# Kernel tuning notes

Measured on AMD Instinct MI355X. Metric: run time of the kernel, lower is better.

Reference implementation:

```python
import jax, jax.numpy as jnp
import numpy as np

N, E, G = 50000, 400000, 2048
H, C = 4, 64            # heads, hidden per head
IN, ED, TASKS = 29, 6, 12
HC = H * C


def setup_inputs() -> dict:
    key = jax.random.key(0)
    ks = jax.random.split(key, 20)
    s = 0.1
    f32 = jnp.float32
    inp = {
        'x': jax.random.normal(ks[0], (N, IN), f32),
        'edge_index': jax.random.randint(ks[1], (2, E), 0, N),
        'edge_attr': jax.random.normal(ks[2], (E, ED), f32),
        'batch': jnp.sort(jax.random.randint(ks[3], (N,), 0, G)),
        # layer 1 (in=29 -> H*C=256)
        'W1': jax.random.normal(ks[4], (IN, HC), f32) * s,
        'as1': jax.random.normal(ks[5], (1, H, C), f32) * s,
        'ad1': jax.random.normal(ks[6], (1, H, C), f32) * s,
        'We1': jax.random.normal(ks[7], (ED, HC), f32) * s,
        'ae1': jax.random.normal(ks[8], (1, H, C), f32) * s,
        'b1': jnp.zeros((HC,), f32),
        # layer 2 (in=256 -> 256)
        'W2': jax.random.normal(ks[9], (HC, HC), f32) * s,
        'as2': jax.random.normal(ks[10], (1, H, C), f32) * s,
        'ad2': jax.random.normal(ks[11], (1, H, C), f32) * s,
        'We2': jax.random.normal(ks[12], (ED, HC), f32) * s,
        'ae2': jax.random.normal(ks[13], (1, H, C), f32) * s,
        'b2': jnp.zeros((HC,), f32),
        # readout linear (256 -> 12)
        'Wl': jax.random.normal(ks[14], (HC, TASKS), f32) * s,
        'bl': jnp.zeros((TASKS,), f32),
    }
    return inp


def _gat_conv(x, src, dst, eattr, W, a_src, a_dst, We, a_e, b):
    """PyG GATConv, concat=True, leaky_relu slope 0.2, self-loops already appended."""
    h = (x @ W).reshape(N, H, C)                      # [N,H,C]
    al_s = jnp.sum(h * a_src, axis=-1)                # [N,H]
    al_d = jnp.sum(h * a_dst, axis=-1)                # [N,H]
    he = (eattr @ We).reshape(-1, H, C)               # [Etot,H,C]
    al_e = jnp.sum(he * a_e, axis=-1)                 # [Etot,H]
    alpha = al_s[src] + al_d[dst] + al_e              # [Etot,H]
    alpha = jax.nn.leaky_relu(alpha, negative_slope=0.2)
    # segment softmax over incoming edges of each dst node
    amax = jax.ops.segment_max(alpha, dst, num_segments=N)
    ex = jnp.exp(alpha - amax[dst])
    denom = jax.ops.segment_sum(ex, dst, num_segments=N)
    alpha = ex / (denom[dst] + 1e-16)
    msg = h[src] * alpha[:, :, None]                  # [Etot,H,C]
    out = jax.ops.segment_sum(msg, dst, num_segments=N)
    return out.reshape(N, HC) + b


def reference(x, edge_index, edge_attr, batch,
              W1, as1, ad1, We1, ae1, b1,
              W2, as2, ad2, We2, ae2, b2, Wl, bl):
    # add self-loops with edge_attr fill = mean over existing edges (PyG default)
    loop = jnp.arange(N)
    src = jnp.concatenate([edge_index[0], loop])
    dst = jnp.concatenate([edge_index[1], loop])
    mean_e = jnp.mean(edge_attr, axis=0, keepdims=True)
    eattr = jnp.concatenate([edge_attr, jnp.broadcast_to(mean_e, (N, ED))], axis=0)

    h = _gat_conv(x, src, dst, eattr, W1, as1, ad1, We1, ae1, b1)
    h = jax.nn.relu(h)
    h = _gat_conv(h, src, dst, eattr, W2, as2, ad2, We2, ae2, b2)
    h = jax.nn.relu(h)

    # global mean pool over graphs
    sums = jax.ops.segment_sum(h, batch, num_segments=G)      # [G,HC]
    cnt = jax.ops.segment_sum(jnp.ones((N,), h.dtype), batch, num_segments=G)
    pooled = sums / jnp.maximum(cnt, 1.0)[:, None]
    return pooled @ Wl + bl
```

## Files before the change

### kernel.cpp

```cpp
#include <hip/hip_runtime.h>
#include <math.h>

static constexpr int NN = 50000;
static constexpr int EE = 400000;
static constexpr int GG = 2048;
static constexpr int TASKS = 12;

typedef __attribute__((ext_vector_type(8))) short short8;
typedef __attribute__((ext_vector_type(4))) float floatx4;

__device__ __forceinline__ unsigned short f2bf(float f) {
  unsigned u = __float_as_uint(f);
  u = u + 0x7fffu + ((u >> 16) & 1u);
  return (unsigned short)(u >> 16);
}
__device__ __forceinline__ float bflo(unsigned u) { return __uint_as_float(u << 16); }
__device__ __forceinline__ float bfhi(unsigned u) { return __uint_as_float(u & 0xffff0000u); }

static constexpr int NBDEG = (EE + 255) / 256;
static constexpr int NBMEAN = 256;
static constexpr int NBX = (NN * 4 + 255) / 256;
static constexpr int NW1 = 32;
static constexpr int NW2 = 256;
__global__ void k_pre(const int* __restrict__ dst, const float* __restrict__ ea,
                      const float* __restrict__ x, const float* __restrict__ W1,
                      const float* __restrict__ W2, int* __restrict__ deg,
                      float* __restrict__ msum, unsigned short* __restrict__ xb,
                      unsigned short* __restrict__ w1t, unsigned short* __restrict__ w2t) {
  const int b = blockIdx.x;
  const int t = threadIdx.x;
  if (b < NBDEG) {
    int e = b * 256 + t;
    if (e < EE) atomicAdd(&deg[dst[e]], 1);
  } else if (b < NBDEG + NBMEAN) {
    float s[6] = {0, 0, 0, 0, 0, 0};
    for (int e = (b - NBDEG) * 256 + t; e < EE; e += NBMEAN * 256) {
#pragma unroll
      for (int d = 0; d < 6; d++) s[d] += ea[(size_t)e * 6 + d];
    }
    __shared__ float ls[6];
    if (t < 6) ls[t] = 0.f;
    __syncthreads();
#pragma unroll
    for (int d = 0; d < 6; d++) atomicAdd(&ls[d], s[d]);
    __syncthreads();
    if (t < 6) atomicAdd(&msum[t], ls[t]);
  } else if (b < NBDEG + NBMEAN + NBX) {
    int i = (b - NBDEG - NBMEAN) * 256 + t;
    if (i < NN * 4) {
      int n = i >> 2, seg = i & 3;
      unsigned short v[8];
#pragma unroll
      for (int j = 0; j < 8; j++) {
        int k = seg * 8 + j;
        v[j] = (k < 29) ? f2bf(x[(size_t)n * 29 + k]) : (unsigned short)0;
      }
      *(short8*)(xb + (size_t)n * 32 + seg * 8) = *(short8*)v;
    }
  } else if (b < NBDEG + NBMEAN + NBX + NW1) {
    int i = (b - NBDEG - NBMEAN - NBX) * 256 + t;
    int row = i >> 5, k = i & 31;
    unsigned short v = (k < 29) ? f2bf(W1[(size_t)k * 256 + row]) : (unsigned short)0;
    w1t[((row >> 4) * 4 + (k >> 3)) * 128 + (row & 15) * 8 + (k & 7)] = v;
  } else {
    int i = (b - NBDEG - NBMEAN - NBX - NW1) * 256 + t;
    int row = i >> 8, k = i & 255;
    w2t[((row >> 4) * 32 + (k >> 3)) * 128 + (row & 15) * 8 + (k & 7)] = f2bf(W2[(size_t)k * 256 + row]);
  }
}

__global__ void k_scan1(const int* __restrict__ deg, int* __restrict__ rowptr, int* __restrict__ bsums) {
  __shared__ int sh[256];
  int i = blockIdx.x * 256 + threadIdx.x;
  int v = (i < NN) ? deg[i] : 0;
  sh[threadIdx.x] = v;
  __syncthreads();
  for (int off = 1; off < 256; off <<= 1) {
    int t = (threadIdx.x >= off) ? sh[threadIdx.x - off] : 0;
    __syncthreads();
    sh[threadIdx.x] += t;
    __syncthreads();
  }
  if (i < NN) rowptr[i] = sh[threadIdx.x] - v;
  if (threadIdx.x == 255) bsums[blockIdx.x] = sh[255];
}

__global__ void k_scan23(int* __restrict__ rowptr, const int* __restrict__ bsums, int nb) {
  __shared__ int sh[256];
  const int t = threadIdx.x;
  sh[t] = (t < nb) ? bsums[t] : 0;
  __syncthreads();
  for (int off = 1; off < 256; off <<= 1) {
    int tv = (t >= off) ? sh[t - off] : 0;
    __syncthreads();
    sh[t] += tv;
    __syncthreads();
  }
  const int add = (blockIdx.x == 0) ? 0 : sh[blockIdx.x - 1];
  int i = blockIdx.x * 256 + t;
  if (i < NN) rowptr[i] += add;
  if (i == 0) rowptr[NN] = EE;
}

template <int KP>
__device__ __forceinline__ void gemm_body(
    int bx, const unsigned short* __restrict__ A, const unsigned short* __restrict__ Bt,
    const float* __restrict__ a_s, const float* __restrict__ a_d,
    unsigned short* __restrict__ Y, float* __restrict__ als, float* __restrict__ ald, int M) {
  const int tid = threadIdx.x;
  const int lane = tid & 63;
  const int w = tid >> 6;
  const int l15 = lane & 15;
  const int quad = lane >> 4;
  const int row0 = bx * 64;

  floatx4 acc[4][4];
#pragma unroll
  for (int i = 0; i < 4; i++)
#pragma unroll
    for (int j = 0; j < 4; j++) acc[i][j] = {0.f, 0.f, 0.f, 0.f};

  const unsigned short* pa[4];
  const unsigned short* pb[4];
#pragma unroll
  for (int i = 0; i < 4; i++) {
    int r = row0 + i * 16 + l15;
    if (r >= M) r = M - 1;
    pa[i] = A + (size_t)r * KP + quad * 8;
  }
#pragma unroll
  for (int j = 0; j < 4; j++)
    pb[j] = Bt + (size_t)((w * 4 + j) * (KP / 8) + quad) * 128 + l15 * 8;

  constexpr int NPH = KP / 32;
  short8 af[2][4], bfr[2][4];
#pragma unroll
  for (int i = 0; i < 4; i++) af[0][i] = *(const short8*)pa[i];
#pragma unroll
  for (int j = 0; j < 4; j++) bfr[0][j] = *(const short8*)pb[j];
#pragma unroll
  for (int ph = 0; ph < NPH; ph++) {
    const int cur = ph & 1, nxt = cur ^ 1;
    if (ph + 1 < NPH) {
#pragma unroll
      for (int i = 0; i < 4; i++) {
        pa[i] += 32;
        af[nxt][i] = *(const short8*)pa[i];
      }
#pragma unroll
      for (int j = 0; j < 4; j++) {
        pb[j] += 512;
        bfr[nxt][j] = *(const short8*)pb[j];
      }
    }
#pragma unroll
    for (int i = 0; i < 4; i++)
#pragma unroll
      for (int j = 0; j < 4; j++)
        acc[i][j] = __builtin_amdgcn_mfma_f32_16x16x32_bf16(af[cur][i], bfr[cur][j], acc[i][j], 0, 0, 0);
  }
  float asc[4], adc[4];
#pragma unroll
  for (int j = 0; j < 4; j++) {
    asc[j] = a_s[w * 64 + j * 16 + l15];
    adc[j] = a_d[w * 64 + j * 16 + l15];
  }
#pragma unroll
  for (int i = 0; i < 4; i++) {
#pragma unroll
    for (int r = 0; r < 4; r++) {
      const int row = row0 + i * 16 + quad * 4 + r;
      unsigned ub[4];
      float hv[4];
#pragma unroll
      for (int j = 0; j < 4; j++) {
        ub[j] = f2bf(acc[i][j][r]);
        hv[j] = __uint_as_float(ub[j] << 16);
      }
      if (row < M) {
#pragma unroll
        for (int j = 0; j < 4; j++) Y[(size_t)row * 256 + w * 64 + j * 16 + l15] = (unsigned short)ub[j];
      }
      float ps = hv[0] * asc[0] + hv[1] * asc[1] + hv[2] * asc[2] + hv[3] * asc[3];
      float pd = hv[0] * adc[0] + hv[1] * adc[1] + hv[2] * adc[2] + hv[3] * adc[3];
#pragma unroll
      for (int off = 1; off < 16; off <<= 1) {
        ps += __shfl_xor(ps, off, 64);
        pd += __shfl_xor(pd, off, 64);
      }
      if (l15 == 0 && row < M) {
        als[row * 4 + w] = ps;
        ald[row * 4 + w] = pd;
      }
    }
  }
}

static constexpr int GB = (NN + 63) / 64;

__global__ __launch_bounds__(256, 2) void k_scatgemm1(
    const int* __restrict__ ei, const int* __restrict__ rowptr, int* __restrict__ cursor,
    int* __restrict__ csrc, int* __restrict__ eslot, const float* __restrict__ We1,
    const float* __restrict__ ae1, const float* __restrict__ We2, const float* __restrict__ ae2,
    const float* __restrict__ msum, float* __restrict__ p1, float* __restrict__ p2,
    const unsigned short* __restrict__ xb, const unsigned short* __restrict__ w1t,
    const float* __restrict__ as1, const float* __restrict__ ad1,
    unsigned short* __restrict__ hb, float* __restrict__ als, float* __restrict__ ald) {
  const int b = blockIdx.x;
  const int t = threadIdx.x;
  if (b < NBDEG) {
    int e = b * 256 + t;
    if (e >= EE) return;
    int s = ei[e];
    int d = ei[EE + e];
    int p = atomicAdd(&cursor[d], 1);
    int slot = rowptr[d] + p;
    csrc[slot] = s;
    eslot[e] = slot;
  } else if (b < NBDEG + 2) {
    const int layer = b - NBDEG;
    const float* We = layer ? We2 : We1;
    const float* ae = layer ? ae2 : ae1;
    float* params = layer ? p2 : p1;
    __shared__ float vsh[24];
    if (t < 24) {
      int d = t >> 2, h = t & 3;
      float s = 0.f;
      for (int c = 0; c < 64; c++) s += We[d * 256 + h * 64 + c] * ae[h * 64 + c];
      vsh[t] = s;
      params[t] = s;
    }
    __syncthreads();
    if (t < 4) {
      float s = 0.f;
      const float invE = 1.0f / (float)EE;
#pragma unroll
      for (int d = 0; d < 6; d++) s += (msum[d] * invE) * vsh[d * 4 + t];
      params[24 + t] = s;
    }
  } else {
    gemm_body<32>(b - NBDEG - 2, xb, w1t, as1, ad1, hb, als, ald, NN);
  }
}

__global__ __launch_bounds__(256, 2) void k_gemm2(
    const unsigned short* __restrict__ A, const unsigned short* __restrict__ Bt,
    const float* __restrict__ a_s, const float* __restrict__ a_d,
    unsigned short* __restrict__ Y, float* __restrict__ als, float* __restrict__ ald) {
  gemm_body<256>(blockIdx.x, A, Bt, a_s, a_d, Y, als, ald, NN);
}

__device__ __forceinline__ float leaky02(float x) { return x > 0.f ? x : 0.2f * x; }

__global__ void k_edge(const int* __restrict__ ei, const float* __restrict__ ea,
                       const float* __restrict__ als, const float* __restrict__ ald,
                       const int* __restrict__ eslot, const float* __restrict__ params,
                       float* __restrict__ exa) {
  int e = blockIdx.x * blockDim.x + threadIdx.x;
  if (e >= EE) return;
  int src = ei[e], dst = ei[EE + e];
  float4 s4 = *(const float4*)(als + (size_t)src * 4);
  float4 d4 = *(const float4*)(ald + (size_t)dst * 4);
  float ed[6];
#pragma unroll
  for (int d = 0; d < 6; d++) ed[d] = ea[(size_t)e * 6 + d];
  float sl[4] = {s4.x + d4.x, s4.y + d4.y, s4.z + d4.z, s4.w + d4.w};
  float out[4];
#pragma unroll
  for (int h = 0; h < 4; h++) {
    float x = sl[h];
#pragma unroll
    for (int d = 0; d < 6; d++) x += ed[d] * params[d * 4 + h];
    out[h] = __expf(leaky02(x));
  }
  *(float4*)(exa + (size_t)eslot[e] * 4) = make_float4(out[0], out[1], out[2], out[3]);
}

__global__ __launch_bounds__(256) void k_agg(
    const unsigned short* __restrict__ hinb, const float* __restrict__ als,
    const float* __restrict__ ald, const int* __restrict__ rowptr, const int* __restrict__ csrc,
    const float* __restrict__ exa, const float* __restrict__ params, const float* __restrict__ bias,
    unsigned short* __restrict__ houtb) {
  const int lane = threadIdx.x & 63;
  const int n = blockIdx.x * 4 + (threadIdx.x >> 6);
  if (n >= NN) return;
  const int half = lane >> 5;
  const int sl = lane & 31;
  const int head = sl >> 3;

  float acc[8];
  float ssum;
  {
    float slg = leaky02(als[n * 4 + head] + ald[n * 4 + head] + params[24 + head]);
    float exs = __expf(slg);
    float wgt = (half == 0) ? exs : 0.f;
    ssum = wgt;
    uint4 uv = *(const uint4*)(hinb + (size_t)n * 256 + sl * 8);
    acc[0] = bflo(uv.x) * wgt;
    acc[1] = bfhi(uv.x) * wgt;
    acc[2] = bflo(uv.y) * wgt;
    acc[3] = bfhi(uv.y) * wgt;
    acc[4] = bflo(uv.z) * wgt;
    acc[5] = bfhi(uv.z) * wgt;
    acc[6] = bflo(uv.w) * wgt;
    acc[7] = bfhi(uv.w) * wgt;
  }
  const int end = rowptr[n + 1];
  int s = rowptr[n] + half;
  int sn1 = 0;
  float ex0 = 0.f, ex1 = 0.f;
  uint4 uv0 = make_uint4(0, 0, 0, 0);
  if (s < end) {
    int sn0 = csrc[s];
    ex0 = exa[(size_t)s * 4 + head];
    uv0 = *(const uint4*)(hinb + (size_t)sn0 * 256 + sl * 8);
  }
  if (s + 2 < end) {
    sn1 = csrc[s + 2];
    ex1 = exa[(size_t)(s + 2) * 4 + head];
  }
  while (s < end) {
    uint4 uvn = make_uint4(0, 0, 0, 0);
    int sn2 = 0;
    float ex2 = 0.f;
    if (s + 2 < end)
      uvn = *(const uint4*)(hinb + (size_t)sn1 * 256 + sl * 8);
    if (s + 4 < end) {
      sn2 = csrc[s + 4];
      ex2 = exa[(size_t)(s + 4) * 4 + head];
    }
    acc[0] += bflo(uv0.x) * ex0;
    acc[1] += bfhi(uv0.x) * ex0;
    acc[2] += bflo(uv0.y) * ex0;
    acc[3] += bfhi(uv0.y) * ex0;
    acc[4] += bflo(uv0.z) * ex0;
    acc[5] += bfhi(uv0.z) * ex0;
    acc[6] += bflo(uv0.w) * ex0;
    acc[7] += bfhi(uv0.w) * ex0;
    ssum += ex0;
    uv0 = uvn;
    ex0 = ex1;
    sn1 = sn2;
    ex1 = ex2;
    s += 2;
  }
#pragma unroll
  for (int j = 0; j < 8; j++) acc[j] += __shfl_xor(acc[j], 32, 64);
  ssum += __shfl_xor(ssum, 32, 64);
  if (half == 0) {
    const float inv = 1.f / (ssum + 1e-16f);
    float4 b0 = *(const float4*)(bias + sl * 8);
    float4 b1 = *(const float4*)(bias + sl * 8 + 4);
    const float bb[8] = {b0.x, b0.y, b0.z, b0.w, b1.x, b1.y, b1.z, b1.w};
    uint p[4];
#pragma unroll
    for (int j = 0; j < 4; j++) {
      float e0 = fmaxf(acc[2 * j] * inv + bb[2 * j], 0.f);
      float e1 = fmaxf(acc[2 * j + 1] * inv + bb[2 * j + 1], 0.f);
      p[j] = (uint)f2bf(e0) | ((uint)f2bf(e1) << 16);
    }
    *(uint4*)(houtb + (size_t)n * 256 + sl * 8) = make_uint4(p[0], p[1], p[2], p[3]);
  }
}

__global__ __launch_bounds__(256) void k_pool(const unsigned short* __restrict__ hb,
                                              const int* __restrict__ batch,
                                              const float* __restrict__ Wl,
                                              const float* __restrict__ bl,
                                              float* __restrict__ out) {
  int g = blockIdx.x;
  int t = threadIdx.x;
  int lo = 0, hi = NN;
  while (lo < hi) {
    int mid = (lo + hi) >> 1;
    if (batch[mid] < g) lo = mid + 1; else hi = mid;
  }
  int start = lo;
  hi = NN;
  while (lo < hi) {
    int mid = (lo + hi) >> 1;
    if (batch[mid] < g + 1) lo = mid + 1; else hi = mid;
  }
  int end = lo;
  const int mid2 = start + ((end - start) >> 1);
  __shared__ float sp[256], sq[256];
  {
    const int c = t & 127;
    const int hseg = t >> 7;
    const int a = hseg ? mid2 : start;
    const int b = hseg ? end : mid2;
    float s0 = 0.f, s1 = 0.f;
    for (int n2 = a; n2 < b; n2++) {
      uint u = ((const uint*)(hb + (size_t)n2 * 256))[c];
      s0 += bflo(u);
      s1 += bfhi(u);
    }
    float* dst = hseg ? sq : sp;
    dst[2 * c] = s0;
    dst[2 * c + 1] = s1;
  }
  __syncthreads();
  if (t < TASKS) {
    float invc = 1.f / fmaxf((float)(end - start), 1.f);
    float o = bl[t];
    for (int c = 0; c < 256; c++) o += (sp[c] + sq[c]) * invc * Wl[c * 12 + t];
    out[(size_t)g * 12 + t] = o;
  }
}

extern "C" void kernel_launch(void* const* d_in, const int* in_sizes, int n_in,
                              void* d_out, int out_size, void* d_ws, size_t ws_size,
                              hipStream_t stream) {
  const float* x = (const float*)d_in[0];
  const int* ei = (const int*)d_in[1];
  const float* ea = (const float*)d_in[2];
  const int* batch = (const int*)d_in[3];
  const float* W1 = (const float*)d_in[4];
  const float* as1 = (const float*)d_in[5];
  const float* ad1 = (const float*)d_in[6];
  const float* We1 = (const float*)d_in[7];
  const float* ae1 = (const float*)d_in[8];
  const float* b1 = (const float*)d_in[9];
  const float* W2 = (const float*)d_in[10];
  const float* as2 = (const float*)d_in[11];
  const float* ad2 = (const float*)d_in[12];
  const float* We2 = (const float*)d_in[13];
  const float* ae2 = (const float*)d_in[14];
  const float* b2 = (const float*)d_in[15];
  const float* Wl = (const float*)d_in[16];
  const float* bl = (const float*)d_in[17];
  float* out = (float*)d_out;

  char* ws = (char*)d_ws;
  size_t off = 0;
  auto take = [&](size_t bytes) -> char* {
    char* p = ws + off;
    off = (off + bytes + 255) & ~(size_t)255;
    return p;
  };
  float* msum = (float*)take(8 * 4);
  int* deg = (int*)take((size_t)NN * 4);
  int* cursor = (int*)take((size_t)NN * 4);
  size_t zero_end = off;
  int* rowptr = (int*)take((size_t)(NN + 1) * 4);
  int* bsums = (int*)take(256 * 4);
  int* csrc = (int*)take((size_t)EE * 4);
  int* eslot = (int*)take((size_t)EE * 4);
  float* exa = (float*)take((size_t)EE * 4 * 4);
  float* p1 = (float*)take(32 * 4);
  float* p2 = (float*)take(32 * 4);
  float* als = (float*)take((size_t)NN * 4 * 4);
  float* ald = (float*)take((size_t)NN * 4 * 4);
  unsigned short* hb = (unsigned short*)take((size_t)NN * 256 * 2);
  unsigned short* ab = (unsigned short*)take((size_t)NN * 256 * 2);
  unsigned short* xb = (unsigned short*)take((size_t)NN * 32 * 2);
  unsigned short* w1t = (unsigned short*)take((size_t)256 * 32 * 2);
  unsigned short* w2t = (unsigned short*)take((size_t)256 * 256 * 2);
  (void)ws_size;

  hipMemsetAsync(ws, 0, zero_end, stream);

  const int nbN = (NN + 255) / 256;
  const int nbE = (EE + 255) / 256;

  k_pre<<<NBDEG + NBMEAN + NBX + NW1 + NW2, 256, 0, stream>>>(ei + EE, ea, x, W1, W2,
                                                              deg, msum, xb, w1t, w2t);
  k_scan1<<<nbN, 256, 0, stream>>>(deg, rowptr, bsums);
  k_scan23<<<nbN, 256, 0, stream>>>(rowptr, bsums, nbN);

  k_scatgemm1<<<NBDEG + 2 + GB, 256, 0, stream>>>(ei, rowptr, cursor, csrc, eslot,
                                                  We1, ae1, We2, ae2, msum, p1, p2,
                                                  xb, w1t, as1, ad1, hb, als, ald);

  k_edge<<<nbE, 256, 0, stream>>>(ei, ea, als, ald, eslot, p1, exa);
  k_agg<<<NN / 4, 256, 0, stream>>>(hb, als, ald, rowptr, csrc, exa, p1, b1, ab);

  k_gemm2<<<GB, 256, 0, stream>>>(ab, w2t, as2, ad2, hb, als, ald);
  k_edge<<<nbE, 256, 0, stream>>>(ei, ea, als, ald, eslot, p2, exa);
  k_agg<<<NN / 4, 256, 0, stream>>>(hb, als, ald, rowptr, csrc, exa, p2, b2, ab);

  k_pool<<<GG, 256, 0, stream>>>(ab, batch, Wl, bl, out);
}
```

Baseline: 312.7 us.

## Fuse two-pass scan into single-pass decoupled lookback and deepen aggregation prefetch

Replaces the two-kernel block scan (local scan, then add block sums) with one kernel that uses decoupled lookback over per-block status flags in zeroed workspace, removing one launch and one pass over rowptr. In the aggregation loop, the gather of neighbour feature rows is now prefetched two iterations ahead instead of one, so more memory loads are in flight. The lookback relies on earlier blocks being scheduled before later ones to avoid spinning forever, and the deeper prefetch adds registers, which may lower occupancy.

```diff
diff --git a/kernel.cpp b/kernel.cpp
--- a/kernel.cpp
+++ b/kernel.cpp
@@ -69,26 +69,15 @@
   }
 }
 
-__global__ void k_scan1(const int* __restrict__ deg, int* __restrict__ rowptr, int* __restrict__ bsums) {
+__global__ void k_scan(const int* __restrict__ deg, int* __restrict__ rowptr,
+                       unsigned* __restrict__ bstate) {
   __shared__ int sh[256];
-  int i = blockIdx.x * 256 + threadIdx.x;
-  int v = (i < NN) ? deg[i] : 0;
-  sh[threadIdx.x] = v;
-  __syncthreads();
-  for (int off = 1; off < 256; off <<= 1) {
-    int t = (threadIdx.x >= off) ? sh[threadIdx.x - off] : 0;
-    __syncthreads();
-    sh[threadIdx.x] += t;
-    __syncthreads();
-  }
-  if (i < NN) rowptr[i] = sh[threadIdx.x] - v;
-  if (threadIdx.x == 255) bsums[blockIdx.x] = sh[255];
-}
-
-__global__ void k_scan23(int* __restrict__ rowptr, const int* __restrict__ bsums, int nb) {
-  __shared__ int sh[256];
+  __shared__ int exc_sh;
+  const int b = blockIdx.x;
   const int t = threadIdx.x;
-  sh[t] = (t < nb) ? bsums[t] : 0;
+  const int i = b * 256 + t;
+  const int v = (i < NN) ? deg[i] : 0;
+  sh[t] = v;
   __syncthreads();
   for (int off = 1; off < 256; off <<= 1) {
     int tv = (t >= off) ? sh[t - off] : 0;
@@ -96,9 +85,32 @@
     sh[t] += tv;
     __syncthreads();
   }
-  const int add = (blockIdx.x == 0) ? 0 : sh[blockIdx.x - 1];
-  int i = blockIdx.x * 256 + t;
-  if (i < NN) rowptr[i] += add;
+  const int total = sh[255];
+  if (t == 0) {
+    if (b == 0) {
+      exc_sh = 0;
+      __hip_atomic_store(&bstate[0], (2u << 30) | (unsigned)total, __ATOMIC_RELEASE,
+                         __HIP_MEMORY_SCOPE_AGENT);
+    } else {
+      __hip_atomic_store(&bstate[b], (1u << 30) | (unsigned)total, __ATOMIC_RELEASE,
+                         __HIP_MEMORY_SCOPE_AGENT);
+      int run = 0;
+      int pb = b - 1;
+      while (true) {
+        unsigned s = __hip_atomic_load(&bstate[pb], __ATOMIC_ACQUIRE, __HIP_MEMORY_SCOPE_AGENT);
+        unsigned flag = s >> 30;
+        if (flag == 0u) continue;
+        run += (int)(s & 0x3FFFFFFFu);
+        if (flag == 2u) break;
+        pb--;
+      }
+      exc_sh = run;
+      __hip_atomic_store(&bstate[b], (2u << 30) | (unsigned)(run + total), __ATOMIC_RELEASE,
+                         __HIP_MEMORY_SCOPE_AGENT);
+    }
+  }
+  __syncthreads();
+  if (i < NN) rowptr[i] = exc_sh + sh[t] - v;
   if (i == 0) rowptr[NN] = EE;
 }
 
@@ -307,41 +319,48 @@
   }
   const int end = rowptr[n + 1];
   int s = rowptr[n] + half;
-  int sn1 = 0;
-  float ex0 = 0.f, ex1 = 0.f;
-  uint4 uv0 = make_uint4(0, 0, 0, 0);
+  int sn2 = 0;
+  float ex0 = 0.f, ex1 = 0.f, ex2 = 0.f;
+  uint4 r0 = make_uint4(0, 0, 0, 0), r1 = make_uint4(0, 0, 0, 0);
   if (s < end) {
     int sn0 = csrc[s];
     ex0 = exa[(size_t)s * 4 + head];
-    uv0 = *(const uint4*)(hinb + (size_t)sn0 * 256 + sl * 8);
+    r0 = *(const uint4*)(hinb + (size_t)sn0 * 256 + sl * 8);
   }
   if (s + 2 < end) {
-    sn1 = csrc[s + 2];
+    int sn1 = csrc[s + 2];
     ex1 = exa[(size_t)(s + 2) * 4 + head];
+    r1 = *(const uint4*)(hinb + (size_t)sn1 * 256 + sl * 8);
+  }
+  if (s + 4 < end) {
+    sn2 = csrc[s + 4];
+    ex2 = exa[(size_t)(s + 4) * 4 + head];
   }
   while (s < end) {
-    uint4 uvn = make_uint4(0, 0, 0, 0);
-    int sn2 = 0;
-    float ex2 = 0.f;
-    if (s + 2 < end)
-      uvn = *(const uint4*)(hinb + (size_t)sn1 * 256 + sl * 8);
-    if (s + 4 < end) {
-      sn2 = csrc[s + 4];
-      ex2 = exa[(size_t)(s + 4) * 4 + head];
-    }
-    acc[0] += bflo(uv0.x) * ex0;
-    acc[1] += bfhi(uv0.x) * ex0;
-    acc[2] += bflo(uv0.y) * ex0;
-    acc[3] += bfhi(uv0.y) * ex0;
-    acc[4] += bflo(uv0.z) * ex0;
-    acc[5] += bfhi(uv0.z) * ex0;
-    acc[6] += bflo(uv0.w) * ex0;
-    acc[7] += bfhi(uv0.w) * ex0;
+    uint4 r2 = make_uint4(0, 0, 0, 0);
+    int sn3 = 0;
+    float ex3 = 0.f;
+    if (s + 4 < end)
+      r2 = *(const uint4*)(hinb + (size_t)sn2 * 256 + sl * 8);
+    if (s + 6 < end) {
+      sn3 = csrc[s + 6];
+      ex3 = exa[(size_t)(s + 6) * 4 + head];
+    }
+    acc[0] += bflo(r0.x) * ex0;
+    acc[1] += bfhi(r0.x) * ex0;
+    acc[2] += bflo(r0.y) * ex0;
+    acc[3] += bfhi(r0.y) * ex0;
+    acc[4] += bflo(r0.z) * ex0;
+    acc[5] += bfhi(r0.z) * ex0;
+    acc[6] += bflo(r0.w) * ex0;
+    acc[7] += bfhi(r0.w) * ex0;
     ssum += ex0;
-    uv0 = uvn;
+    r0 = r1;
+    r1 = r2;
     ex0 = ex1;
-    sn1 = sn2;
     ex1 = ex2;
+    ex2 = ex3;
+    sn2 = sn3;
     s += 2;
   }
 #pragma unroll
@@ -441,9 +460,9 @@
   float* msum = (float*)take(8 * 4);
   int* deg = (int*)take((size_t)NN * 4);
   int* cursor = (int*)take((size_t)NN * 4);
+  unsigned* bstate = (unsigned*)take(256 * 4);
   size_t zero_end = off;
   int* rowptr = (int*)take((size_t)(NN + 1) * 4);
-  int* bsums = (int*)take(256 * 4);
   int* csrc = (int*)take((size_t)EE * 4);
   int* eslot = (int*)take((size_t)EE * 4);
   float* exa = (float*)take((size_t)EE * 4 * 4);
@@ -465,8 +484,7 @@
 
   k_pre<<<NBDEG + NBMEAN + NBX + NW1 + NW2, 256, 0, stream>>>(ei + EE, ea, x, W1, W2,
                                                               deg, msum, xb, w1t, w2t);
-  k_scan1<<<nbN, 256, 0, stream>>>(deg, rowptr, bsums);
-  k_scan23<<<nbN, 256, 0, stream>>>(rowptr, bsums, nbN);
+  k_scan<<<nbN, 256, 0, stream>>>(deg, rowptr, bstate);
 
   k_scatgemm1<<<NBDEG + 2 + GB, 256, 0, stream>>>(ei, rowptr, cursor, csrc, eslot,
                                                   We1, ae1, We2, ae2, msum, p1, p2,
```

After: 348.4 us. +11.4%, slower.
